# Optimization experiments

Measured on AMD Instinct MI355X. Metric: run time of the kernel, lower is better.

Reference implementation:

```python
import jax, jax.numpy as jnp
import numpy as np

N = 20000
MOL = 16
MH = 64      # message_hidden
UH = 64      # update_hidden
HEADS = 2
CUTOFF = 0.02257
E_FIX = 720000
REL_IN = 3 + 2 + MOL          # 21
SELF_F = 2 + MOL + 1 + 1      # 20
EDGE_A = MH + SELF_F          # 84
OUT_D = 2 + 1 + MOL + 1       # 20


def _build_edges(x_np, cutoff):
    """All ordered pairs (i,j), i!=j, with dist<=cutoff (matches symmetrized triu in torch)."""
    src_l, dst_l = [], []
    chunk = 1000
    Nn = x_np.shape[0]
    c2 = cutoff * cutoff
    for i0 in range(0, Nn, chunk):
        xi = x_np[i0:i0 + chunk]
        d2 = ((xi[:, None, :] - x_np[None, :, :]) ** 2).sum(-1)
        ii, jj = np.nonzero(d2 <= c2)
        ii = ii + i0
        keep = ii != jj
        dst_l.append(ii[keep])
        src_l.append(jj[keep])
    return (np.concatenate(src_l).astype(np.int32),
            np.concatenate(dst_l).astype(np.int32))


def setup_inputs() -> dict:
    key = jax.random.key(0)
    ks = jax.random.split(key, 30)
    x = jax.random.uniform(ks[0], (N, 2), dtype=jnp.float32)
    angle = jax.random.normal(ks[1], (N, 1), dtype=jnp.float32)
    molecules = jax.random.normal(ks[2], (N, MOL), dtype=jnp.float32)
    generation = jnp.zeros((N, 1), dtype=jnp.float32)

    src_np, dst_np = _build_edges(np.asarray(x), CUTOFF)
    E = min(src_np.shape[0], E_FIX)
    src = np.zeros(E_FIX, np.int32)
    dst = np.zeros(E_FIX, np.int32)
    mask = np.zeros(E_FIX, np.float32)
    src[:E] = src_np[:E]
    dst[:E] = dst_np[:E]
    mask[:E] = 1.0

    def p(k, shape):
        return jax.random.normal(k, shape, dtype=jnp.float32) * 0.05

    inp = dict(
        x=x, angle=angle, molecules=molecules, generation=generation,
        src=jnp.asarray(src), dst=jnp.asarray(dst), edge_mask=jnp.asarray(mask),
        # message_mlp
        mw1=p(ks[3], (REL_IN, MH)), mb1=p(ks[4], (MH,)),
        mw2=p(ks[5], (MH, MH)), mb2=p(ks[6], (MH,)),
        mw3=p(ks[7], (MH, MH)), mb3=p(ks[8], (MH,)),
        # TransformerConv (heads=2, out=UH, concat=False, edge_dim=EDGE_A)
        wq=p(ks[9], (SELF_F, HEADS * UH)), bq=p(ks[10], (HEADS * UH,)),
        wk=p(ks[11], (SELF_F, HEADS * UH)), bk=p(ks[12], (HEADS * UH,)),
        wv=p(ks[13], (SELF_F, HEADS * UH)), bv=p(ks[14], (HEADS * UH,)),
        we=p(ks[15], (EDGE_A, HEADS * UH)),  # lin_edge has no bias in PyG
        wskip=p(ks[16], (SELF_F, UH)), bskip=p(ks[17], (UH,)),
        # node_head
        hw1=p(ks[18], (UH, UH)), hb1=p(ks[19], (UH,)),
        hw2=p(ks[20], (UH, UH)), hb2=p(ks[21], (UH,)),
        hw3=p(ks[22], (UH, OUT_D)), hb3=p(ks[23], (OUT_D,)),
    )
    return inp


def reference(x, angle, molecules, generation, src, dst, edge_mask,
              mw1, mb1, mw2, mb2, mw3, mb3,
              wq, bq, wk, bk, wv, bv, we, wskip, bskip,
              hw1, hb1, hw2, hb2, hw3, hb3):
    Nn = x.shape[0]
    H, C = HEADS, UH
    m = edge_mask  # [E], 1 for real edges, 0 for padding

    # relative edge features (j = src = neighbor, i = dst = center)
    dxdy = x[src] - x[dst]                                          # [E,2]
    r = jnp.sqrt(jnp.clip((dxdy ** 2).sum(-1, keepdims=True), 1e-12))
    d_ang = angle[src] - angle[dst]                                 # [E,1]
    d_mol = molecules[src] - molecules[dst]                         # [E,MOL]
    rel_in = jnp.concatenate([dxdy, r, jnp.sin(d_ang), jnp.cos(d_ang), d_mol], -1)

    h = jax.nn.relu(rel_in @ mw1 + mb1)
    h = jax.nn.relu(h @ mw2 + mb2)
    msg = jax.nn.relu(h @ mw3 + mb3)                                # [E,MH]

    degree = jax.ops.segment_sum(m, dst, num_segments=Nn)[:, None]  # [N,1]
    self_feat = jnp.concatenate(
        [jnp.sin(angle), jnp.cos(angle), molecules, generation, degree], -1)  # [N,20]
    edge_attr = jnp.concatenate([msg, self_feat[dst]], -1)          # [E,84]

    # TransformerConv: q_i, (k_j + e), (v_j + e); per-dst segment softmax; mean heads; + skip
    q = (self_feat @ wq + bq).reshape(Nn, H, C)
    k = (self_feat @ wk + bk).reshape(Nn, H, C)
    v = (self_feat @ wv + bv).reshape(Nn, H, C)
    e = (edge_attr @ we).reshape(-1, H, C)
    key_e = k[src] + e
    val_e = v[src] + e
    alpha = (q[dst] * key_e).sum(-1) / jnp.sqrt(jnp.float32(C))     # [E,H]
    alpha = jnp.where(m[:, None] > 0, alpha, -1e9)
    amax = jax.ops.segment_max(alpha, dst, num_segments=Nn)         # [N,H]
    ex = jnp.exp(alpha - amax[dst]) * m[:, None]
    denom = jax.ops.segment_sum(ex, dst, num_segments=Nn)           # [N,H]
    w = ex / (denom[dst] + 1e-16)                                   # [E,H]
    out = jax.ops.segment_sum(val_e * w[:, :, None], dst, num_segments=Nn)  # [N,H,C]
    out = out.mean(axis=1) + (self_feat @ wskip + bskip)            # [N,UH]

    u = jax.nn.relu(out @ hw1 + hb1)
    u = jax.nn.relu(u @ hw2 + hb2)
    upd = u @ hw3 + hb3                                             # [N,20]

    return (upd[:, 0:2], upd[:, 2:3], upd[:, 3:3 + MOL], upd[:, 3 + MOL:4 + MOL])
```

## Files before the change

### kernel.cpp

```cpp
#include <hip/hip_runtime.h>
#include <hip/hip_bf16.h>
#include <math.h>

#define NN 20000
#define EF 720000

typedef float  f4 __attribute__((ext_vector_type(4)));
typedef unsigned int u4 __attribute__((ext_vector_type(4)));

__device__ __forceinline__ void MFMA(f4& c, u4 a, u4 b) {
    asm("v_mfma_f32_16x16x32_bf16 %0, %1, %2, %0" : "+v"(c) : "v"(a), "v"(b));
}

__device__ __forceinline__ unsigned pk(float a, float b) {
    __hip_bfloat162 t = __halves2bfloat162(__float2bfloat16(a), __float2bfloat16(b));
    unsigned u; __builtin_memcpy(&u, &t, 4); return u;
}
__device__ __forceinline__ float bf2f(unsigned short u) {
    return __builtin_bit_cast(float, (unsigned)u << 16);
}
__device__ __forceinline__ unsigned short f2bfu(float f) {
    __hip_bfloat16 b = __float2bfloat16(f);
    unsigned short u; __builtin_memcpy(&u, &b, 2); return u;
}

__global__ __launch_bounds__(256) void k_prep(
    const float* __restrict__ mw1, const float* __restrict__ mb1,
    const float* __restrict__ mw2, const float* __restrict__ mw3,
    const float* __restrict__ hw1, const float* __restrict__ hw2, const float* __restrict__ hw3,
    const float* __restrict__ we, const float* __restrict__ wk, const float* __restrict__ bk,
    const float* __restrict__ wv, const float* __restrict__ bv,
    const float* __restrict__ wq, const float* __restrict__ bq,
    __hip_bfloat16* __restrict__ W1b, __hip_bfloat16* __restrict__ W2b, __hip_bfloat16* __restrict__ W3b,
    __hip_bfloat16* __restrict__ H1b, __hip_bfloat16* __restrict__ H2b, __hip_bfloat16* __restrict__ H3b,
    __hip_bfloat16* __restrict__ WcA, float* __restrict__ Mwe, float* __restrict__ Mk)
{
    int t = blockIdx.x * 256 + threadIdx.x;
    if (t < 2048) {
        int ch = t >> 5, k = t & 31;
        float v = (k < 21) ? mw1[k * 64 + ch] : (k == 21 ? mb1[ch] : 0.f);
        W1b[t] = __float2bfloat16(v); return;
    }
    t -= 2048;
    if (t < 4096) { int ch = t >> 6, k = t & 63; W2b[t] = __float2bfloat16(mw2[k * 64 + ch]); return; }
    t -= 4096;
    if (t < 4096) { int ch = t >> 6, k = t & 63; W3b[t] = __float2bfloat16(mw3[k * 64 + ch]); return; }
    t -= 4096;
    if (t < 4096) { int ch = t >> 6, k = t & 63; H1b[t] = __float2bfloat16(hw1[k * 64 + ch]); return; }
    t -= 4096;
    if (t < 4096) { int ch = t >> 6, k = t & 63; H2b[t] = __float2bfloat16(hw2[k * 64 + ch]); return; }
    t -= 4096;
    if (t < 2048) {
        int ch = t >> 6, k = t & 63;
        float v = (ch < 20) ? hw3[k * 20 + ch] : 0.f;
        H3b[t] = __float2bfloat16(v); return;
    }
    t -= 2048;
    if (t < 16384) {
        int h = t >> 13, rem = t & 8191;
        int ch = rem >> 7, k = rem & 127;
        int col = h * 64 + ch;
        float v;
        if (k < 64)        v = we[k * 128 + col];
        else if (k < 84)   v = wv[(k - 64) * 128 + col];
        else if (k == 84)  v = bv[col];
        else if (k < 96)   v = 0.f;
        else if (k < 116)  v = we[(64 + (k - 96)) * 128 + col];
        else               v = 0.f;
        WcA[t] = __float2bfloat16(v); return;
    }
    t -= 16384;
    if (t < 4032) {
        int j = t / 192, o = t % 192;
        int h = (o >= 96) ? 1 : 0, a = o - 96 * h;
        float acc = 0.f;
        if (a < 84) {
            for (int c = 0; c < 64; c++) {
                int hc = h * 64 + c;
                float wqv = (j < 20) ? wq[j * 128 + hc] : bq[hc];
                acc += wqv * we[a * 128 + hc];
            }
        }
        Mwe[t] = acc; return;
    }
    t -= 4032;
    if (t < 1344) {
        int j = t / 64, rem = t % 64;
        int h = rem >> 5, a = rem & 31;
        float acc = 0.f;
        if (a <= 20) {
            for (int c = 0; c < 64; c++) {
                int hc = h * 64 + c;
                float wqv = (j < 20) ? wq[j * 128 + hc] : bq[hc];
                float wkv = (a < 20) ? wk[a * 128 + hc] : bk[hc];
                acc += wqv * wkv;
            }
        }
        Mk[t] = acc; return;
    }
}

__global__ __launch_bounds__(256) void k_csr(
    const int* __restrict__ dst, const float* __restrict__ mask, int* __restrict__ row_off)
{
    int n = blockIdx.x * 256 + threadIdx.x;
    if (n > NN) return;
    int lo = 0, hi = EF;
    while (lo < hi) { int mid = (lo + hi) >> 1; if (mask[mid] > 0.5f) lo = mid + 1; else hi = mid; }
    int Ea = lo;
    lo = 0; hi = Ea;
    while (lo < hi) { int mid = (lo + hi) >> 1; if (dst[mid] < n) lo = mid + 1; else hi = mid; }
    row_off[n] = lo;
}

__global__ __launch_bounds__(256) void k_node(
    const float* __restrict__ angle, const float* __restrict__ mol, const float* __restrict__ gen,
    const int* __restrict__ row_off,
    const float* __restrict__ wskip, const float* __restrict__ bskip,
    const float* __restrict__ Mwe, const float* __restrict__ Mk,
    float* __restrict__ selff, __hip_bfloat16* __restrict__ selffb,
    float* __restrict__ skipf, float* __restrict__ qwe, float* __restrict__ qkp)
{
    int wid = threadIdx.x >> 6, lane = threadIdx.x & 63;
    int n = blockIdx.x * 4 + wid;

    float an = angle[n];
    float sv, cv; sincosf(an, &sv, &cv);
    float degf = (float)(row_off[n + 1] - row_off[n]);
    float sfa[21];
    sfa[0] = sv; sfa[1] = cv;
#pragma unroll
    for (int j = 0; j < 16; j++) sfa[2 + j] = mol[n * 16 + j];
    sfa[18] = gen[n];
    sfa[19] = degf;
    sfa[20] = 1.f;

    float sval = (lane == 0) ? sv : (lane == 1) ? cv :
                 (lane < 18) ? mol[n * 16 + (lane - 2)] :
                 (lane == 18) ? gen[n] : degf;
    if (lane < 20) selff[n * 20 + lane] = sval;
    if (lane < 32) {
        float v = (lane < 20) ? sval : (lane == 20 ? 1.f : 0.f);
        selffb[n * 32 + lane] = __float2bfloat16(v);
    }

    float sk = bskip[lane];
#pragma unroll
    for (int j = 0; j < 20; j++) sk += sfa[j] * wskip[j * 64 + lane];
    skipf[n * 64 + lane] = sk;

#pragma unroll
    for (int r = 0; r < 3; r++) {
        int o = r * 64 + lane;
        float acc = 0.f;
#pragma unroll
        for (int j = 0; j < 21; j++) acc += sfa[j] * Mwe[j * 192 + o];
        qwe[n * 192 + o] = acc;
    }

    {
        float acc = 0.f;
#pragma unroll
        for (int j = 0; j < 21; j++) acc += sfa[j] * Mk[j * 64 + lane];
        qkp[n * 64 + lane] = acc;
    }
}

__device__ __forceinline__ void write_tiles(char* lds, int l, f4 (&acc)[4][4], const float* bias)
{
#pragma unroll
    for (int m = 0; m < 4; m++) {
        f4 bv;
        if (bias) bv = *(const f4*)(bias + m * 16 + ((l >> 4) << 2));
        else      { bv.x = 0.f; bv.y = 0.f; bv.z = 0.f; bv.w = 0.f; }
#pragma unroll
        for (int n = 0; n < 4; n++) {
            f4 v = acc[m][n];
            float v0 = fmaxf(v.x + bv.x, 0.f);
            float v1 = fmaxf(v.y + bv.y, 0.f);
            float v2 = fmaxf(v.z + bv.z, 0.f);
            float v3 = fmaxf(v.w + bv.w, 0.f);
            int e   = n * 16 + (l & 15);
            int ch0 = m * 16 + ((l >> 4) << 2);
            int byte = e * 128 + ((((ch0 >> 3) ^ (e & 7))) << 4) + (ch0 & 7) * 2;
            uint2 w; w.x = pk(v0, v1); w.y = pk(v2, v3);
            *(uint2*)(lds + byte) = w;
        }
    }
}

__global__ __launch_bounds__(256) void k_edge_mfma(
    const float* __restrict__ x, const float* __restrict__ angle, const float* __restrict__ mol,
    const int* __restrict__ src, const int* __restrict__ dst,
    const float* __restrict__ mask,
    const __hip_bfloat16* __restrict__ W1b, const __hip_bfloat16* __restrict__ W2b,
    const __hip_bfloat16* __restrict__ W3b,
    const float* __restrict__ mb2, const float* __restrict__ mb3,
    __hip_bfloat16* __restrict__ msg)
{
    __shared__ char lds_all[4][64 * 128];
    int wv = threadIdx.x >> 6, l = threadIdx.x & 63;
    char* lds = lds_all[wv];
    int e0 = (blockIdx.x * 4 + wv) * 64;
    if (e0 + 64 > EF) e0 = EF - 64;

    if (mask[e0] < 0.5f) return;

    int s = src[e0 + l], d = dst[e0 + l];
    float2 xs = ((const float2*)x)[s], xd = ((const float2*)x)[d];
    float dx = xs.x - xd.x, dy = xs.y - xd.y;
    float r = sqrtf(fmaxf(dx * dx + dy * dy, 1e-12f));
    float da = angle[s] - angle[d];
    float sv, cv; sincosf(da, &sv, &cv);
    const float4* m4 = (const float4*)mol;
    float4 sa = m4[s * 4 + 0], sb = m4[s * 4 + 1], sc = m4[s * 4 + 2], sd = m4[s * 4 + 3];
    float4 ta = m4[d * 4 + 0], tb = m4[d * 4 + 1], tc = m4[d * 4 + 2], td = m4[d * 4 + 3];
    float f[22];
    f[0] = dx; f[1] = dy; f[2] = r; f[3] = sv; f[4] = cv;
    f[5]  = sa.x - ta.x; f[6]  = sa.y - ta.y; f[7]  = sa.z - ta.z; f[8]  = sa.w - ta.w;
    f[9]  = sb.x - tb.x; f[10] = sb.y - tb.y; f[11] = sb.z - tb.z; f[12] = sb.w - tb.w;
    f[13] = sc.x - tc.x; f[14] = sc.y - tc.y; f[15] = sc.z - tc.z; f[16] = sc.w - tc.w;
    f[17] = sd.x - td.x; f[18] = sd.y - td.y; f[19] = sd.z - td.z; f[20] = sd.w - td.w;
    f[21] = 1.f;
    unsigned p[16];
#pragma unroll
    for (int j = 0; j < 11; j++) p[j] = pk(f[2 * j], f[2 * j + 1]);
#pragma unroll
    for (int j = 11; j < 16; j++) p[j] = 0u;
#pragma unroll
    for (int g = 0; g < 4; g++) {
        int byte = l * 64 + ((g ^ (l & 3)) << 4);
        u4 w; w.x = p[4 * g]; w.y = p[4 * g + 1]; w.z = p[4 * g + 2]; w.w = p[4 * g + 3];
        *(u4*)(lds + byte) = w;
    }

    u4 B1[4];
#pragma unroll
    for (int n = 0; n < 4; n++) {
        int e = n * 16 + (l & 15);
        int byte = e * 64 + ((((l >> 4) & 3) ^ (e & 3)) << 4);
        B1[n] = *(const u4*)(lds + byte);
    }

    f4 acc[4][4];
#pragma unroll
    for (int m = 0; m < 4; m++)
#pragma unroll
        for (int n = 0; n < 4; n++) { acc[m][n].x = 0.f; acc[m][n].y = 0.f; acc[m][n].z = 0.f; acc[m][n].w = 0.f; }

    const unsigned short* W1u = (const unsigned short*)W1b;
    const unsigned short* W2u = (const unsigned short*)W2b;
    const unsigned short* W3u = (const unsigned short*)W3b;
#pragma unroll
    for (int m = 0; m < 4; m++) {
        u4 w = *(const u4*)(W1u + (m * 16 + (l & 15)) * 32 + (l >> 4) * 8);
#pragma unroll
        for (int n = 0; n < 4; n++) MFMA(acc[m][n], w, B1[n]);
    }
    write_tiles(lds, l, acc, nullptr);

    u4 B2[4][2];
#pragma unroll
    for (int n = 0; n < 4; n++)
#pragma unroll
        for (int ks = 0; ks < 2; ks++) {
            int e = n * 16 + (l & 15);
            int g = ks * 4 + (l >> 4);
            B2[n][ks] = *(const u4*)(lds + e * 128 + ((g ^ (e & 7)) << 4));
        }
#pragma unroll
    for (int m = 0; m < 4; m++)
#pragma unroll
        for (int n = 0; n < 4; n++) { acc[m][n].x = 0.f; acc[m][n].y = 0.f; acc[m][n].z = 0.f; acc[m][n].w = 0.f; }
#pragma unroll
    for (int m = 0; m < 4; m++)
#pragma unroll
        for (int ks = 0; ks < 2; ks++) {
            u4 w = *(const u4*)(W2u + (m * 16 + (l & 15)) * 64 + ks * 32 + (l >> 4) * 8);
#pragma unroll
            for (int n = 0; n < 4; n++) MFMA(acc[m][n], w, B2[n][ks]);
        }
    write_tiles(lds, l, acc, mb2);

#pragma unroll
    for (int n = 0; n < 4; n++)
#pragma unroll
        for (int ks = 0; ks < 2; ks++) {
            int e = n * 16 + (l & 15);
            int g = ks * 4 + (l >> 4);
            B2[n][ks] = *(const u4*)(lds + e * 128 + ((g ^ (e & 7)) << 4));
        }
#pragma unroll
    for (int m = 0; m < 4; m++)
#pragma unroll
        for (int n = 0; n < 4; n++) { acc[m][n].x = 0.f; acc[m][n].y = 0.f; acc[m][n].z = 0.f; acc[m][n].w = 0.f; }
#pragma unroll
    for (int m = 0; m < 4; m++)
#pragma unroll
        for (int ks = 0; ks < 2; ks++) {
            u4 w = *(const u4*)(W3u + (m * 16 + (l & 15)) * 64 + ks * 32 + (l >> 4) * 8);
#pragma unroll
            for (int n = 0; n < 4; n++) MFMA(acc[m][n], w, B2[n][ks]);
        }
    write_tiles(lds, l, acc, mb3);

#pragma unroll
    for (int it = 0; it < 8; it++) {
        int e = it * 8 + (l >> 3);
        int g = l & 7;
        u4 vv = *(const u4*)(lds + e * 128 + ((g ^ (e & 7)) << 4));
        *(u4*)((unsigned short*)msg + (size_t)(e0 + e) * 64 + g * 8) = vv;
    }
}

__global__ __launch_bounds__(256) void k_attn(
    const int* __restrict__ row_off, const int* __restrict__ src,
    const __hip_bfloat16* __restrict__ msg,
    const __hip_bfloat16* __restrict__ selffb, const float* __restrict__ qkp,
    const float* __restrict__ qwe, const float* __restrict__ selff,
    __hip_bfloat16* __restrict__ agg, float* __restrict__ invp)
{
    int tid = threadIdx.x, wid = tid >> 6, lane = tid & 63;
    int g = lane >> 3, c8 = lane & 7;
    int n = blockIdx.x * 4 + wid;

    const float* qrow = qwe + (size_t)n * 192;
    f4 qmA0 = *(const f4*)(qrow + 8 * c8);
    f4 qmA1 = *(const f4*)(qrow + 8 * c8 + 4);
    f4 qmB0 = *(const f4*)(qrow + 96 + 8 * c8);
    f4 qmB1 = *(const f4*)(qrow + 96 + 8 * c8 + 4);
    float qk0a = qkp[n * 64 + c8],      qk0b = qkp[n * 64 + c8 + 8],      qk0c = qkp[n * 64 + c8 + 16];
    float qk1a = qkp[n * 64 + 32 + c8], qk1b = qkp[n * 64 + 32 + c8 + 8], qk1c = qkp[n * 64 + 32 + c8 + 16];

    float a00 = 0.f, a01 = 0.f;
#pragma unroll
    for (int j = 0; j < 20; j++) {
        float sfj = selff[n * 20 + j];
        a00 += sfj * qrow[64 + j];
        a01 += sfj * qrow[96 + 64 + j];
    }

    const unsigned short* msgu = (const unsigned short*)msg;
    const unsigned short* sfu  = (const unsigned short*)selffb;
    int r0 = row_off[n], r1 = row_off[n + 1];
    int nit = (r1 - r0 + 7) >> 3;

    f4 WmA0 = {0,0,0,0}, WmA1 = {0,0,0,0}, WmB0 = {0,0,0,0}, WmB1 = {0,0,0,0};
    float Ws0a = 0.f, Ws0b = 0.f, Ws0c = 0.f, Ws1a = 0.f, Ws1b = 0.f, Ws1c = 0.f;
    float S0 = 0.f, S1 = 0.f;

#pragma unroll 2
    for (int it = 0; it < nit; it++) {
        int e = r0 + it * 8 + g;
        bool ok = (e < r1);
        int ec = ok ? e : r0;
        int s = src[ec];
        float sfA = bf2f(sfu[(size_t)s * 32 + c8]);
        float sfB = bf2f(sfu[(size_t)s * 32 + c8 + 8]);
        float sfC = bf2f(sfu[(size_t)s * 32 + c8 + 16]);
        u4 mr = *(const u4*)(msgu + (size_t)ec * 64 + 8 * c8);
        float c0 = __builtin_bit_cast(float, mr.x << 16);
        float c1 = __builtin_bit_cast(float, mr.x & 0xffff0000u);
        float c2 = __builtin_bit_cast(float, mr.y << 16);
        float c3 = __builtin_bit_cast(float, mr.y & 0xffff0000u);
        float c4 = __builtin_bit_cast(float, mr.z << 16);
        float c5 = __builtin_bit_cast(float, mr.z & 0xffff0000u);
        float c6 = __builtin_bit_cast(float, mr.w << 16);
        float c7 = __builtin_bit_cast(float, mr.w & 0xffff0000u);

        float t0 = qmA0.x * c0 + qmA0.y * c1 + qmA0.z * c2 + qmA0.w * c3
                 + qmA1.x * c4 + qmA1.y * c5 + qmA1.z * c6 + qmA1.w * c7
                 + sfA * qk0a + sfB * qk0b + sfC * qk0c;
        float t1 = qmB0.x * c0 + qmB0.y * c1 + qmB0.z * c2 + qmB0.w * c3
                 + qmB1.x * c4 + qmB1.y * c5 + qmB1.z * c6 + qmB1.w * c7
                 + sfA * qk1a + sfB * qk1b + sfC * qk1c;
#pragma unroll
        for (int mk = 1; mk < 8; mk <<= 1) {
            t0 += __shfl_xor(t0, mk, 64);
            t1 += __shfl_xor(t1, mk, 64);
        }
        float w0 = ok ? __expf((t0 + a00) * 0.125f) : 0.f;
        float w1 = ok ? __expf((t1 + a01) * 0.125f) : 0.f;
        S0 += w0; S1 += w1;
        WmA0.x += w0 * c0; WmA0.y += w0 * c1; WmA0.z += w0 * c2; WmA0.w += w0 * c3;
        WmA1.x += w0 * c4; WmA1.y += w0 * c5; WmA1.z += w0 * c6; WmA1.w += w0 * c7;
        WmB0.x += w1 * c0; WmB0.y += w1 * c1; WmB0.z += w1 * c2; WmB0.w += w1 * c3;
        WmB1.x += w1 * c4; WmB1.y += w1 * c5; WmB1.z += w1 * c6; WmB1.w += w1 * c7;
        Ws0a += w0 * sfA; Ws0b += w0 * sfB; Ws0c += w0 * sfC;
        Ws1a += w1 * sfA; Ws1b += w1 * sfB; Ws1c += w1 * sfC;
    }

#pragma unroll
    for (int mk = 8; mk <= 32; mk <<= 1) {
        WmA0.x += __shfl_xor(WmA0.x, mk, 64); WmA0.y += __shfl_xor(WmA0.y, mk, 64);
        WmA0.z += __shfl_xor(WmA0.z, mk, 64); WmA0.w += __shfl_xor(WmA0.w, mk, 64);
        WmA1.x += __shfl_xor(WmA1.x, mk, 64); WmA1.y += __shfl_xor(WmA1.y, mk, 64);
        WmA1.z += __shfl_xor(WmA1.z, mk, 64); WmA1.w += __shfl_xor(WmA1.w, mk, 64);
        WmB0.x += __shfl_xor(WmB0.x, mk, 64); WmB0.y += __shfl_xor(WmB0.y, mk, 64);
        WmB0.z += __shfl_xor(WmB0.z, mk, 64); WmB0.w += __shfl_xor(WmB0.w, mk, 64);
        WmB1.x += __shfl_xor(WmB1.x, mk, 64); WmB1.y += __shfl_xor(WmB1.y, mk, 64);
        WmB1.z += __shfl_xor(WmB1.z, mk, 64); WmB1.w += __shfl_xor(WmB1.w, mk, 64);
        Ws0a += __shfl_xor(Ws0a, mk, 64); Ws0b += __shfl_xor(Ws0b, mk, 64); Ws0c += __shfl_xor(Ws0c, mk, 64);
        Ws1a += __shfl_xor(Ws1a, mk, 64); Ws1b += __shfl_xor(Ws1b, mk, 64); Ws1c += __shfl_xor(Ws1c, mk, 64);
        S0 += __shfl_xor(S0, mk, 64); S1 += __shfl_xor(S1, mk, 64);
    }

    unsigned short* arow = (unsigned short*)agg + (size_t)n * 256;
    if (g == 0) {
        u4 w; w.x = pk(WmA0.x, WmA0.y); w.y = pk(WmA0.z, WmA0.w);
        w.z = pk(WmA1.x, WmA1.y); w.w = pk(WmA1.z, WmA1.w);
        *(u4*)(arow + 8 * c8) = w;
    } else if (g == 1) {
        u4 w; w.x = pk(WmB0.x, WmB0.y); w.y = pk(WmB0.z, WmB0.w);
        w.z = pk(WmB1.x, WmB1.y); w.w = pk(WmB1.z, WmB1.w);
        *(u4*)(arow + 128 + 8 * c8) = w;
    } else if (g == 2) {
        arow[64 + c8]      = f2bfu(Ws0a);
        arow[64 + c8 + 8]  = f2bfu(Ws0b);
        arow[64 + c8 + 16] = f2bfu(Ws0c);
    } else if (g == 3) {
        arow[128 + 64 + c8]      = f2bfu(Ws1a);
        arow[128 + 64 + c8 + 8]  = f2bfu(Ws1b);
        arow[128 + 64 + c8 + 16] = f2bfu(Ws1c);
    } else if (g == 4) {
        arow[96 + c8]     = f2bfu(S0 * selff[n * 20 + c8]);
        arow[96 + c8 + 8] = f2bfu(S0 * selff[n * 20 + c8 + 8]);
        if (c8 < 4) arow[96 + c8 + 16] = f2bfu(S0 * selff[n * 20 + c8 + 16]);
    } else if (g == 5) {
        arow[128 + 96 + c8]     = f2bfu(S1 * selff[n * 20 + c8]);
        arow[128 + 96 + c8 + 8] = f2bfu(S1 * selff[n * 20 + c8 + 8]);
        if (c8 < 4) arow[128 + 96 + c8 + 16] = f2bfu(S1 * selff[n * 20 + c8 + 16]);
    } else if (g == 6 && c8 == 0) {
        invp[2 * n]     = 1.f / (S0 + 1e-16f);
        invp[2 * n + 1] = 1.f / (S1 + 1e-16f);
    }
}

__global__ __launch_bounds__(64) void k_final2(
    const __hip_bfloat16* __restrict__ agg, const float* __restrict__ invp,
    const float* __restrict__ skipf, const __hip_bfloat16* __restrict__ WcA,
    const __hip_bfloat16* __restrict__ H1b, const __hip_bfloat16* __restrict__ H2b,
    const __hip_bfloat16* __restrict__ H3b,
    const float* __restrict__ hb1, const float* __restrict__ hb2, const float* __restrict__ hb3,
    float* __restrict__ out)
{
    __shared__ char lds[64 * 128];
    int l = threadIdx.x;
    int n0 = blockIdx.x * 64;

    const unsigned short* aggU = (const unsigned short*)agg;
    const unsigned short* WcU = (const unsigned short*)WcA;
    const unsigned short* H1u = (const unsigned short*)H1b;
    const unsigned short* H2u = (const unsigned short*)H2b;
    const unsigned short* H3u = (const unsigned short*)H3b;

    int nodes[4];
    float inv0[4], inv1[4];
#pragma unroll
    for (int n4 = 0; n4 < 4; n4++) {
        int node = n0 + n4 * 16 + (l & 15); if (node >= NN) node = NN - 1;
        nodes[n4] = node;
        float2 iv = *(const float2*)(invp + 2 * node);
        inv0[n4] = iv.x; inv1[n4] = iv.y;
    }

    f4 osum[4][4];
#pragma unroll
    for (int m = 0; m < 4; m++)
#pragma unroll
        for (int n4 = 0; n4 < 4; n4++) { osum[m][n4].x = 0.f; osum[m][n4].y = 0.f; osum[m][n4].z = 0.f; osum[m][n4].w = 0.f; }

#pragma unroll
    for (int h = 0; h < 2; h++) {
        f4 acc[4][4];
#pragma unroll
        for (int m = 0; m < 4; m++)
#pragma unroll
            for (int n4 = 0; n4 < 4; n4++) { acc[m][n4].x = 0.f; acc[m][n4].y = 0.f; acc[m][n4].z = 0.f; acc[m][n4].w = 0.f; }
#pragma unroll
        for (int ks = 0; ks < 4; ks++) {
            u4 A[4];
#pragma unroll
            for (int m = 0; m < 4; m++)
                A[m] = *(const u4*)(WcU + h * 8192 + (m * 16 + (l & 15)) * 128 + ks * 32 + (l >> 4) * 8);
#pragma unroll
            for (int n4 = 0; n4 < 4; n4++) {
                u4 B = *(const u4*)(aggU + (size_t)nodes[n4] * 256 + h * 128 + ks * 32 + (l >> 4) * 8);
#pragma unroll
                for (int m = 0; m < 4; m++) MFMA(acc[m][n4], A[m], B);
            }
        }
        const float* iv = h ? inv1 : inv0;
#pragma unroll
        for (int m = 0; m < 4; m++)
#pragma unroll
            for (int n4 = 0; n4 < 4; n4++) {
                float s = 0.5f * iv[n4];
                osum[m][n4].x += s * acc[m][n4].x; osum[m][n4].y += s * acc[m][n4].y;
                osum[m][n4].z += s * acc[m][n4].z; osum[m][n4].w += s * acc[m][n4].w;
            }
    }

#pragma unroll
    for (int m = 0; m < 4; m++) {
#pragma unroll
        for (int n4 = 0; n4 < 4; n4++) {
            int ch0 = m * 16 + ((l >> 4) << 2);
            float4 sk = *(const float4*)(skipf + (size_t)nodes[n4] * 64 + ch0);
            f4 v = osum[m][n4];
            float v0 = v.x + sk.x, v1 = v.y + sk.y, v2 = v.z + sk.z, v3 = v.w + sk.w;
            int e = n4 * 16 + (l & 15);
            int byte = e * 128 + ((((ch0 >> 3) ^ (e & 7))) << 4) + (ch0 & 7) * 2;
            uint2 w; w.x = pk(v0, v1); w.y = pk(v2, v3);
            *(uint2*)(lds + byte) = w;
        }
    }
    __syncthreads();

    u4 B[4][2];
    f4 acc[4][4];

#pragma unroll
    for (int n = 0; n < 4; n++)
#pragma unroll
        for (int ks = 0; ks < 2; ks++) {
            int e = n * 16 + (l & 15);
            int g = ks * 4 + (l >> 4);
            B[n][ks] = *(const u4*)(lds + e * 128 + ((g ^ (e & 7)) << 4));
        }
    __syncthreads();
#pragma unroll
    for (int m = 0; m < 4; m++)
#pragma unroll
        for (int n = 0; n < 4; n++) { acc[m][n].x = 0.f; acc[m][n].y = 0.f; acc[m][n].z = 0.f; acc[m][n].w = 0.f; }
#pragma unroll
    for (int m = 0; m < 4; m++)
#pragma unroll
        for (int ks = 0; ks < 2; ks++) {
            u4 w = *(const u4*)(H1u + (m * 16 + (l & 15)) * 64 + ks * 32 + (l >> 4) * 8);
#pragma unroll
            for (int n = 0; n < 4; n++) MFMA(acc[m][n], w, B[n][ks]);
        }
    write_tiles(lds, l, acc, hb1);
    __syncthreads();

#pragma unroll
    for (int n = 0; n < 4; n++)
#pragma unroll
        for (int ks = 0; ks < 2; ks++) {
            int e = n * 16 + (l & 15);
            int g = ks * 4 + (l >> 4);
            B[n][ks] = *(const u4*)(lds + e * 128 + ((g ^ (e & 7)) << 4));
        }
    __syncthreads();
#pragma unroll
    for (int m = 0; m < 4; m++)
#pragma unroll
        for (int n = 0; n < 4; n++) { acc[m][n].x = 0.f; acc[m][n].y = 0.f; acc[m][n].z = 0.f; acc[m][n].w = 0.f; }
#pragma unroll
    for (int m = 0; m < 4; m++)
#pragma unroll
        for (int ks = 0; ks < 2; ks++) {
            u4 w = *(const u4*)(H2u + (m * 16 + (l & 15)) * 64 + ks * 32 + (l >> 4) * 8);
#pragma unroll
            for (int n = 0; n < 4; n++) MFMA(acc[m][n], w, B[n][ks]);
        }
    write_tiles(lds, l, acc, hb2);
    __syncthreads();

#pragma unroll
    for (int n = 0; n < 4; n++)
#pragma unroll
        for (int ks = 0; ks < 2; ks++) {
            int e = n * 16 + (l & 15);
            int g = ks * 4 + (l >> 4);
            B[n][ks] = *(const u4*)(lds + e * 128 + ((g ^ (e & 7)) << 4));
        }

    f4 acc3[2][4];
#pragma unroll
    for (int m = 0; m < 2; m++)
#pragma unroll
        for (int n = 0; n < 4; n++) { acc3[m][n].x = 0.f; acc3[m][n].y = 0.f; acc3[m][n].z = 0.f; acc3[m][n].w = 0.f; }
#pragma unroll
    for (int m = 0; m < 2; m++)
#pragma unroll
        for (int ks = 0; ks < 2; ks++) {
            u4 w = *(const u4*)(H3u + (m * 16 + (l & 15)) * 64 + ks * 32 + (l >> 4) * 8);
#pragma unroll
            for (int n = 0; n < 4; n++) MFMA(acc3[m][n], w, B[n][ks]);
        }

#pragma unroll
    for (int m = 0; m < 2; m++) {
#pragma unroll
        for (int j = 0; j < 4; j++) {
            int ch = m * 16 + (l >> 4) * 4 + j;
            if (ch < 20) {
                float b = hb3[ch];
#pragma unroll
                for (int nt = 0; nt < 4; nt++) {
                    int node = n0 + nt * 16 + (l & 15);
                    if (node < NN) {
                        float v = acc3[m][nt][j] + b;
                        if (ch < 2)       out[node * 2 + ch] = v;
                        else if (ch == 2) out[2 * NN + node] = v;
                        else if (ch < 19) out[3 * NN + node * 16 + (ch - 3)] = v;
                        else              out[19 * NN + node] = v;
                    }
                }
            }
        }
    }
}

extern "C" void kernel_launch(void* const* d_in, const int* in_sizes, int n_in,
                              void* d_out, int out_size, void* d_ws, size_t ws_size,
                              hipStream_t stream)
{
    const float* x      = (const float*)d_in[0];
    const float* angle  = (const float*)d_in[1];
    const float* mol    = (const float*)d_in[2];
    const float* gen    = (const float*)d_in[3];
    const int*   src    = (const int*)d_in[4];
    const int*   dst    = (const int*)d_in[5];
    const float* mask   = (const float*)d_in[6];
    const float* mw1    = (const float*)d_in[7];
    const float* mb1    = (const float*)d_in[8];
    const float* mw2    = (const float*)d_in[9];
    const float* mb2    = (const float*)d_in[10];
    const float* mw3    = (const float*)d_in[11];
    const float* mb3    = (const float*)d_in[12];
    const float* wq     = (const float*)d_in[13];
    const float* bq     = (const float*)d_in[14];
    const float* wk     = (const float*)d_in[15];
    const float* bk     = (const float*)d_in[16];
    const float* wv     = (const float*)d_in[17];
    const float* bv     = (const float*)d_in[18];
    const float* we     = (const float*)d_in[19];
    const float* wskip  = (const float*)d_in[20];
    const float* bskip  = (const float*)d_in[21];
    const float* hw1    = (const float*)d_in[22];
    const float* hb1    = (const float*)d_in[23];
    const float* hw2    = (const float*)d_in[24];
    const float* hb2    = (const float*)d_in[25];
    const float* hw3    = (const float*)d_in[26];
    const float* hb3    = (const float*)d_in[27];
    float* out = (float*)d_out;

    char* p = (char*)d_ws;
    auto alloc = [&](size_t bytes) -> void* {
        void* r = (void*)p;
        p += (bytes + 255) & ~(size_t)255;
        return r;
    };
    int*   row_off = (int*)alloc((NN + 1) * 4);
    float* selff   = (float*)alloc((size_t)NN * 20 * 4);
    __hip_bfloat16* selffb = (__hip_bfloat16*)alloc((size_t)NN * 32 * 2);
    float* qkp     = (float*)alloc((size_t)NN * 64 * 4);
    float* skipf   = (float*)alloc((size_t)NN * 64 * 4);
    float* qwe     = (float*)alloc((size_t)NN * 192 * 4);
    __hip_bfloat16* agg = (__hip_bfloat16*)alloc((size_t)NN * 256 * 2);
    float* invp    = (float*)alloc((size_t)NN * 2 * 4);
    __hip_bfloat16* W1b = (__hip_bfloat16*)alloc(2048 * 2);
    __hip_bfloat16* W2b = (__hip_bfloat16*)alloc(4096 * 2);
    __hip_bfloat16* W3b = (__hip_bfloat16*)alloc(4096 * 2);
    __hip_bfloat16* H1b = (__hip_bfloat16*)alloc(4096 * 2);
    __hip_bfloat16* H2b = (__hip_bfloat16*)alloc(4096 * 2);
    __hip_bfloat16* H3b = (__hip_bfloat16*)alloc(2048 * 2);
    __hip_bfloat16* WcA = (__hip_bfloat16*)alloc(16384 * 2);
    float* Mwe     = (float*)alloc(4032 * 4);
    float* Mk      = (float*)alloc(1344 * 4);
    __hip_bfloat16* msg = (__hip_bfloat16*)alloc((size_t)EF * 64 * 2);

    k_prep<<<165, 256, 0, stream>>>(mw1, mb1, mw2, mw3, hw1, hw2, hw3, we, wk, bk, wv, bv,
                                    wq, bq, W1b, W2b, W3b, H1b, H2b, H3b, WcA, Mwe, Mk);
    k_csr<<<(NN + 256) / 256, 256, 0, stream>>>(dst, mask, row_off);
    k_node<<<NN / 4, 256, 0, stream>>>(angle, mol, gen, row_off,
                                       wskip, bskip, Mwe, Mk,
                                       selff, selffb, skipf, qwe, qkp);
    k_edge_mfma<<<(EF / 64 + 3) / 4, 256, 0, stream>>>(x, angle, mol, src, dst, mask,
                                                       W1b, W2b, W3b, mb2, mb3, msg);
    k_attn<<<NN / 4, 256, 0, stream>>>(row_off, src, msg, selffb, qkp,
                                       qwe, selff, agg, invp);
    k_final2<<<(NN + 63) / 64, 64, 0, stream>>>(agg, invp, skipf, WcA,
                                                H1b, H2b, H3b, hb1, hb2, hb3, out);
}
```

Baseline: 146.4 us.

## Vectorize attention gathers, precompute per-node bias dot, write messages directly

The attention kernel now gathers source self-features as one 4-wide bf16 load per lane instead of three scalar loads, and reads the query-key projection as vectors. The per-node self-feature dot products move into the node kernel as a shuffle reduction stored in a small buffer, which lets the fp32 self-feature array be dropped. The edge MLP's last layer writes bias+ReLU bf16 results straight from the MFMA accumulators to global memory, skipping the LDS round trip. The direct stores are 8-byte scattered writes rather than coalesced 16-byte rows. The c8 channel mapping also changes from strided to contiguous, which relies on the matching layout in the node-side weights.

Result: no change. 147.5 us (+0.7%).

```diff
diff --git a/kernel.cpp b/kernel.cpp
--- a/kernel.cpp
+++ b/kernel.cpp
@@ -19,9 +19,11 @@
 __device__ __forceinline__ float bf2f(unsigned short u) {
     return __builtin_bit_cast(float, (unsigned)u << 16);
 }
-__device__ __forceinline__ unsigned short f2bfu(float f) {
-    __hip_bfloat16 b = __float2bfloat16(f);
-    unsigned short u; __builtin_memcpy(&u, &b, 2); return u;
+__device__ __forceinline__ f4 bf2f4(ushort4 u) {
+    f4 r; r.x = bf2f(u.x); r.y = bf2f(u.y); r.z = bf2f(u.z); r.w = bf2f(u.w); return r;
+}
+__device__ __forceinline__ float dot4(f4 a, f4 b) {
+    return a.x * b.x + a.y * b.y + a.z * b.z + a.w * b.w;
 }
 
 __global__ __launch_bounds__(256) void k_prep(
@@ -118,8 +120,9 @@
     const int* __restrict__ row_off,
     const float* __restrict__ wskip, const float* __restrict__ bskip,
     const float* __restrict__ Mwe, const float* __restrict__ Mk,
-    float* __restrict__ selff, __hip_bfloat16* __restrict__ selffb,
-    float* __restrict__ skipf, float* __restrict__ qwe, float* __restrict__ qkp)
+    __hip_bfloat16* __restrict__ selffb,
+    float* __restrict__ skipf, float* __restrict__ qwe, float* __restrict__ qkp,
+    float* __restrict__ anode)
 {
     int wid = threadIdx.x >> 6, lane = threadIdx.x & 63;
     int n = blockIdx.x * 4 + wid;
@@ -135,13 +138,12 @@
     sfa[19] = degf;
     sfa[20] = 1.f;
 
-    float sval = (lane == 0) ? sv : (lane == 1) ? cv :
-                 (lane < 18) ? mol[n * 16 + (lane - 2)] :
-                 (lane == 18) ? gen[n] : degf;
-    if (lane < 20) selff[n * 20 + lane] = sval;
     if (lane < 32) {
-        float v = (lane < 20) ? sval : (lane == 20 ? 1.f : 0.f);
-        selffb[n * 32 + lane] = __float2bfloat16(v);
+        float sval = (lane == 0) ? sv : (lane == 1) ? cv :
+                     (lane < 18) ? mol[n * 16 + (lane - 2)] :
+                     (lane == 18) ? gen[n] : (lane == 19) ? degf :
+                     (lane == 20) ? 1.f : 0.f;
+        selffb[n * 32 + lane] = __float2bfloat16(sval);
     }
 
     float sk = bskip[lane];
@@ -149,6 +151,7 @@
     for (int j = 0; j < 20; j++) sk += sfa[j] * wskip[j * 64 + lane];
     skipf[n * 64 + lane] = sk;
 
+    float a00p = 0.f, a01p = 0.f;
 #pragma unroll
     for (int r = 0; r < 3; r++) {
         int o = r * 64 + lane;
@@ -156,7 +159,15 @@
 #pragma unroll
         for (int j = 0; j < 21; j++) acc += sfa[j] * Mwe[j * 192 + o];
         qwe[n * 192 + o] = acc;
-    }
+        if (r == 1 && lane < 20) a00p = sfa[lane] * acc;
+        if (r == 2 && lane >= 32 && lane < 52) a01p = sfa[lane - 32] * acc;
+    }
+#pragma unroll
+    for (int mk = 1; mk < 64; mk <<= 1) {
+        a00p += __shfl_xor(a00p, mk, 64);
+        a01p += __shfl_xor(a01p, mk, 64);
+    }
+    if (lane == 0) { anode[2 * n] = a00p; anode[2 * n + 1] = a01p; }
 
     {
         float acc = 0.f;
@@ -302,14 +313,22 @@
 #pragma unroll
             for (int n = 0; n < 4; n++) MFMA(acc[m][n], w, B2[n][ks]);
         }
-    write_tiles(lds, l, acc, mb3);
-
-#pragma unroll
-    for (int it = 0; it < 8; it++) {
-        int e = it * 8 + (l >> 3);
-        int g = l & 7;
-        u4 vv = *(const u4*)(lds + e * 128 + ((g ^ (e & 7)) << 4));
-        *(u4*)((unsigned short*)msg + (size_t)(e0 + e) * 64 + g * 8) = vv;
+
+#pragma unroll
+    for (int m = 0; m < 4; m++) {
+        f4 bv = *(const f4*)(mb3 + m * 16 + ((l >> 4) << 2));
+#pragma unroll
+        for (int n = 0; n < 4; n++) {
+            f4 v = acc[m][n];
+            float v0 = fmaxf(v.x + bv.x, 0.f);
+            float v1 = fmaxf(v.y + bv.y, 0.f);
+            float v2 = fmaxf(v.z + bv.z, 0.f);
+            float v3 = fmaxf(v.w + bv.w, 0.f);
+            int e   = n * 16 + (l & 15);
+            int ch0 = m * 16 + ((l >> 4) << 2);
+            uint2 w; w.x = pk(v0, v1); w.y = pk(v2, v3);
+            *(uint2*)((unsigned short*)msg + (size_t)(e0 + e) * 64 + ch0) = w;
+        }
     }
 }
 
@@ -317,7 +336,7 @@
     const int* __restrict__ row_off, const int* __restrict__ src,
     const __hip_bfloat16* __restrict__ msg,
     const __hip_bfloat16* __restrict__ selffb, const float* __restrict__ qkp,
-    const float* __restrict__ qwe, const float* __restrict__ selff,
+    const float* __restrict__ qwe, const float* __restrict__ anode,
     __hip_bfloat16* __restrict__ agg, float* __restrict__ invp)
 {
     int tid = threadIdx.x, wid = tid >> 6, lane = tid & 63;
@@ -329,24 +348,20 @@
     f4 qmA1 = *(const f4*)(qrow + 8 * c8 + 4);
     f4 qmB0 = *(const f4*)(qrow + 96 + 8 * c8);
     f4 qmB1 = *(const f4*)(qrow + 96 + 8 * c8 + 4);
-    float qk0a = qkp[n * 64 + c8],      qk0b = qkp[n * 64 + c8 + 8],      qk0c = qkp[n * 64 + c8 + 16];
-    float qk1a = qkp[n * 64 + 32 + c8], qk1b = qkp[n * 64 + 32 + c8 + 8], qk1c = qkp[n * 64 + 32 + c8 + 16];
-
-    float a00 = 0.f, a01 = 0.f;
-#pragma unroll
-    for (int j = 0; j < 20; j++) {
-        float sfj = selff[n * 20 + j];
-        a00 += sfj * qrow[64 + j];
-        a01 += sfj * qrow[96 + 64 + j];
-    }
+    f4 qk0 = *(const f4*)(qkp + n * 64 + 4 * c8);
+    f4 qk1 = *(const f4*)(qkp + n * 64 + 32 + 4 * c8);
+    float2 av = *(const float2*)(anode + 2 * n);
+    float a00 = av.x, a01 = av.y;
 
     const unsigned short* msgu = (const unsigned short*)msg;
     const unsigned short* sfu  = (const unsigned short*)selffb;
+    f4 sfd = bf2f4(*(const ushort4*)(sfu + (size_t)n * 32 + 4 * c8));
+
     int r0 = row_off[n], r1 = row_off[n + 1];
     int nit = (r1 - r0 + 7) >> 3;
 
     f4 WmA0 = {0,0,0,0}, WmA1 = {0,0,0,0}, WmB0 = {0,0,0,0}, WmB1 = {0,0,0,0};
-    float Ws0a = 0.f, Ws0b = 0.f, Ws0c = 0.f, Ws1a = 0.f, Ws1b = 0.f, Ws1c = 0.f;
+    f4 Ws0 = {0,0,0,0}, Ws1 = {0,0,0,0};
     float S0 = 0.f, S1 = 0.f;
 
 #pragma unroll 2
@@ -355,9 +370,7 @@
         bool ok = (e < r1);
         int ec = ok ? e : r0;
         int s = src[ec];
-        float sfA = bf2f(sfu[(size_t)s * 32 + c8]);
-        float sfB = bf2f(sfu[(size_t)s * 32 + c8 + 8]);
-        float sfC = bf2f(sfu[(size_t)s * 32 + c8 + 16]);
+        f4 sfv = bf2f4(*(const ushort4*)(sfu + (size_t)s * 32 + 4 * c8));
         u4 mr = *(const u4*)(msgu + (size_t)ec * 64 + 8 * c8);
         float c0 = __builtin_bit_cast(float, mr.x << 16);
         float c1 = __builtin_bit_cast(float, mr.x & 0xffff0000u);
@@ -370,10 +383,10 @@
 
         float t0 = qmA0.x * c0 + qmA0.y * c1 + qmA0.z * c2 + qmA0.w * c3
                  + qmA1.x * c4 + qmA1.y * c5 + qmA1.z * c6 + qmA1.w * c7
-                 + sfA * qk0a + sfB * qk0b + sfC * qk0c;
+                 + dot4(sfv, qk0);
         float t1 = qmB0.x * c0 + qmB0.y * c1 + qmB0.z * c2 + qmB0.w * c3
                  + qmB1.x * c4 + qmB1.y * c5 + qmB1.z * c6 + qmB1.w * c7
-                 + sfA * qk1a + sfB * qk1b + sfC * qk1c;
+                 + dot4(sfv, qk1);
 #pragma unroll
         for (int mk = 1; mk < 8; mk <<= 1) {
             t0 += __shfl_xor(t0, mk, 64);
@@ -386,8 +399,8 @@
         WmA1.x += w0 * c4; WmA1.y += w0 * c5; WmA1.z += w0 * c6; WmA1.w += w0 * c7;
         WmB0.x += w1 * c0; WmB0.y += w1 * c1; WmB0.z += w1 * c2; WmB0.w += w1 * c3;
         WmB1.x += w1 * c4; WmB1.y += w1 * c5; WmB1.z += w1 * c6; WmB1.w += w1 * c7;
-        Ws0a += w0 * sfA; Ws0b += w0 * sfB; Ws0c += w0 * sfC;
-        Ws1a += w1 * sfA; Ws1b += w1 * sfB; Ws1c += w1 * sfC;
+        Ws0.x += w0 * sfv.x; Ws0.y += w0 * sfv.y; Ws0.z += w0 * sfv.z; Ws0.w += w0 * sfv.w;
+        Ws1.x += w1 * sfv.x; Ws1.y += w1 * sfv.y; Ws1.z += w1 * sfv.z; Ws1.w += w1 * sfv.w;
     }
 
 #pragma unroll
@@ -400,8 +413,10 @@
         WmB0.z += __shfl_xor(WmB0.z, mk, 64); WmB0.w += __shfl_xor(WmB0.w, mk, 64);
         WmB1.x += __shfl_xor(WmB1.x, mk, 64); WmB1.y += __shfl_xor(WmB1.y, mk, 64);
         WmB1.z += __shfl_xor(WmB1.z, mk, 64); WmB1.w += __shfl_xor(WmB1.w, mk, 64);
-        Ws0a += __shfl_xor(Ws0a, mk, 64); Ws0b += __shfl_xor(Ws0b, mk, 64); Ws0c += __shfl_xor(Ws0c, mk, 64);
-        Ws1a += __shfl_xor(Ws1a, mk, 64); Ws1b += __shfl_xor(Ws1b, mk, 64); Ws1c += __shfl_xor(Ws1c, mk, 64);
+        Ws0.x += __shfl_xor(Ws0.x, mk, 64); Ws0.y += __shfl_xor(Ws0.y, mk, 64);
+        Ws0.z += __shfl_xor(Ws0.z, mk, 64); Ws0.w += __shfl_xor(Ws0.w, mk, 64);
+        Ws1.x += __shfl_xor(Ws1.x, mk, 64); Ws1.y += __shfl_xor(Ws1.y, mk, 64);
+        Ws1.z += __shfl_xor(Ws1.z, mk, 64); Ws1.w += __shfl_xor(Ws1.w, mk, 64);
         S0 += __shfl_xor(S0, mk, 64); S1 += __shfl_xor(S1, mk, 64);
     }
 
@@ -415,21 +430,17 @@
         w.z = pk(WmB1.x, WmB1.y); w.w = pk(WmB1.z, WmB1.w);
         *(u4*)(arow + 128 + 8 * c8) = w;
     } else if (g == 2) {
-        arow[64 + c8]      = f2bfu(Ws0a);
-        arow[64 + c8 + 8]  = f2bfu(Ws0b);
-        arow[64 + c8 + 16] = f2bfu(Ws0c);
+        uint2 w; w.x = pk(Ws0.x, Ws0.y); w.y = pk(Ws0.z, Ws0.w);
+        *(uint2*)(arow + 64 + 4 * c8) = w;
     } else if (g == 3) {
-        arow[128 + 64 + c8]      = f2bfu(Ws1a);
-        arow[128 + 64 + c8 + 8]  = f2bfu(Ws1b);
-        arow[128 + 64 + c8 + 16] = f2bfu(Ws1c);
+        uint2 w; w.x = pk(Ws1.x, Ws1.y); w.y = pk(Ws1.z, Ws1.w);
+        *(uint2*)(arow + 128 + 64 + 4 * c8) = w;
     } else if (g == 4) {
-        arow[96 + c8]     = f2bfu(S0 * selff[n * 20 + c8]);
-        arow[96 + c8 + 8] = f2bfu(S0 * selff[n * 20 + c8 + 8]);
-        if (c8 < 4) arow[96 + c8 + 16] = f2bfu(S0 * selff[n * 20 + c8 + 16]);
+        uint2 w; w.x = pk(S0 * sfd.x, S0 * sfd.y); w.y = pk(S0 * sfd.z, S0 * sfd.w);
+        *(uint2*)(arow + 96 + 4 * c8) = w;
     } else if (g == 5) {
-        arow[128 + 96 + c8]     = f2bfu(S1 * selff[n * 20 + c8]);
-        arow[128 + 96 + c8 + 8] = f2bfu(S1 * selff[n * 20 + c8 + 8]);
-        if (c8 < 4) arow[128 + 96 + c8 + 16] = f2bfu(S1 * selff[n * 20 + c8 + 16]);
+        uint2 w; w.x = pk(S1 * sfd.x, S1 * sfd.y); w.y = pk(S1 * sfd.z, S1 * sfd.w);
+        *(uint2*)(arow + 128 + 96 + 4 * c8) = w;
     } else if (g == 6 && c8 == 0) {
         invp[2 * n]     = 1.f / (S0 + 1e-16f);
         invp[2 * n + 1] = 1.f / (S1 + 1e-16f);
@@ -655,11 +666,11 @@
         return r;
     };
     int*   row_off = (int*)alloc((NN + 1) * 4);
-    float* selff   = (float*)alloc((size_t)NN * 20 * 4);
     __hip_bfloat16* selffb = (__hip_bfloat16*)alloc((size_t)NN * 32 * 2);
     float* qkp     = (float*)alloc((size_t)NN * 64 * 4);
     float* skipf   = (float*)alloc((size_t)NN * 64 * 4);
     float* qwe     = (float*)alloc((size_t)NN * 192 * 4);
+    float* anode   = (float*)alloc((size_t)NN * 2 * 4);
     __hip_bfloat16* agg = (__hip_bfloat16*)alloc((size_t)NN * 256 * 2);
     float* invp    = (float*)alloc((size_t)NN * 2 * 4);
     __hip_bfloat16* W1b = (__hip_bfloat16*)alloc(2048 * 2);
@@ -678,11 +689,11 @@
     k_csr<<<(NN + 256) / 256, 256, 0, stream>>>(dst, mask, row_off);
     k_node<<<NN / 4, 256, 0, stream>>>(angle, mol, gen, row_off,
                                        wskip, bskip, Mwe, Mk,
-                                       selff, selffb, skipf, qwe, qkp);
+                                       selffb, skipf, qwe, qkp, anode);
     k_edge_mfma<<<(EF / 64 + 3) / 4, 256, 0, stream>>>(x, angle, mol, src, dst, mask,
                                                        W1b, W2b, W3b, mb2, mb3, msg);
     k_attn<<<NN / 4, 256, 0, stream>>>(row_off, src, msg, selffb, qkp,
-                                       qwe, selff, agg, invp);
+                                       qwe, anode, agg, invp);
     k_final2<<<(NN + 63) / 64, 64, 0, stream>>>(agg, invp, skipf, WcA,
                                                 H1b, H2b, H3b, hb1, hb2, hb3, out);
 }
```
